# Performance work log

Measured on AMD Instinct MI355X. Metric: run time of the kernel, lower is better.

## Reference

```python
import jax, jax.numpy as jnp
import numpy as np

N, D_IN, D_OUT = 16384, 1024, 1024
E, R, TOP_K = 8, 16, 2
ALPHA = 32.0
SCALING = ALPHA / R  # standard LoRA scaling alpha/rank


def setup_inputs() -> dict:
    key = jax.random.key(0)
    k_tok, k_wb, k_a, k_b, k_g = jax.random.split(key, 5)
    tokens = jax.random.normal(k_tok, (N, D_IN), dtype=jnp.float32)
    # frozen attention projection
    W_base = jax.random.normal(k_wb, (D_IN, D_OUT), dtype=jnp.float32) * (1.0 / np.sqrt(D_IN))
    # per-expert LoRA factors
    A = jax.random.normal(k_a, (E, D_IN, R), dtype=jnp.float32) * 0.02
    B = jax.random.normal(k_b, (E, R, D_OUT), dtype=jnp.float32) * 0.02
    # router
    W_gate = jax.random.normal(k_g, (D_IN, E), dtype=jnp.float32) * (1.0 / np.sqrt(D_IN))
    return {"tokens": tokens, "W_base": W_base, "A": A, "B": B, "W_gate": W_gate}


def reference(tokens, W_base, A, B, W_gate):
    # Router: top-k gating with softmax over the selected logits
    router_logits = tokens @ W_gate                      # [N, E]
    topk_vals, selected_experts = jax.lax.top_k(router_logits, TOP_K)  # [N, K]
    expert_weights = jax.nn.softmax(topk_vals, axis=-1)  # [N, K]

    # Dense combine weights: zeros except selected experts
    gates = jnp.zeros((tokens.shape[0], E), dtype=tokens.dtype)
    gates = gates.at[jnp.arange(tokens.shape[0])[:, None], selected_experts].set(expert_weights)  # [N, E]

    # Frozen base projection
    base_out = tokens @ W_base                           # [N, D_out]

    # LoRA experts: low-rank intermediate [N, E, R] is small (rank 16)
    h = jnp.einsum('nd,edr->ner', tokens, A)             # [N, E, R]
    h = h * gates[:, :, None]                            # gate before expanding to D_out
    lora_out = jnp.einsum('ner,erm->nm', h, B)           # [N, D_out]

    out = base_out + SCALING * lora_out
    return out, router_logits, selected_experts, expert_weights
```

## Files before the change

kernel.cpp:

```cpp
#include <hip/hip_runtime.h>
#include <hip/hip_bf16.h>
#include <cstdint>
#include <cfloat>

#define NTOK 16384
#define DIN  1024
#define DOUT 1024
#define NEXP 8
#define RLORA 16
#define KTOT 1152
#define SCALE_LORA 2.0f

typedef __attribute__((ext_vector_type(8))) short bf16x8;
typedef __attribute__((ext_vector_type(4))) float f32x4;

__device__ __forceinline__ unsigned short f2bf(float f) {
  __hip_bfloat16 h = __float2bfloat16(f);
  unsigned short u;
  __builtin_memcpy(&u, &h, 2);
  return u;
}

__device__ __forceinline__ void gld_lds16(const void* g, void* l) {
  __builtin_amdgcn_global_load_lds((const __attribute__((address_space(1))) void*)g,
                                   (__attribute__((address_space(3))) void*)l,
                                   16, 0, 0);
}

__global__ __launch_bounds__(256) void k_prep(const float* __restrict__ Wb,
                                              const float* __restrict__ B,
                                              const float* __restrict__ A,
                                              const float* __restrict__ Wg,
                                              unsigned short* __restrict__ WcatT,
                                              unsigned short* __restrict__ AcatT,
                                              float* __restrict__ WgT) {
  __shared__ unsigned short Tbuf[256 * 17];
  const int bid = blockIdx.x;
  const int t = threadIdx.x;
  if (bid < 288) {
    unsigned short (*T)[66] = (unsigned short (*)[66])Tbuf;
    const int k0 = (bid % 18) * 64, j0 = (bid / 18) * 64;
#pragma unroll
    for (int p = 0; p < 4; ++p) {
      int kk = p * 16 + (t >> 4);
      int c4 = (t & 15) * 4;
      int k = k0 + kk;
      const float* src = (k < 1024) ? (Wb + (size_t)k * 1024) : (B + (size_t)(k - 1024) * 1024);
      float4 v = *(const float4*)(src + j0 + c4);
      T[kk][c4 + 0] = f2bf(v.x); T[kk][c4 + 1] = f2bf(v.y);
      T[kk][c4 + 2] = f2bf(v.z); T[kk][c4 + 3] = f2bf(v.w);
    }
    __syncthreads();
#pragma unroll
    for (int p = 0; p < 2; ++p) {
      int jj = p * 32 + (t >> 3);
      int kc = (t & 7) * 8;
      unsigned short buf[8];
#pragma unroll
      for (int i = 0; i < 8; ++i) buf[i] = T[kc + i][jj];
      uint4 u; __builtin_memcpy(&u, buf, 16);
      *(uint4*)(WcatT + (size_t)(j0 + jj) * KTOT + k0 + kc) = u;
    }
  } else if (bid < 320) {
    unsigned short (*T)[17] = (unsigned short (*)[17])Tbuf;
    const int e = (bid - 288) >> 2, d0 = ((bid - 288) & 3) * 256;
#pragma unroll
    for (int p = 0; p < 4; ++p) {
      int idx = p * 256 + t;
      int d = idx >> 2;
      int rr = (idx & 3) * 4;
      float4 v = *(const float4*)(A + (size_t)e * 16384 + (size_t)(d0 + d) * 16 + rr);
      T[d][rr + 0] = f2bf(v.x); T[d][rr + 1] = f2bf(v.y);
      T[d][rr + 2] = f2bf(v.z); T[d][rr + 3] = f2bf(v.w);
    }
    __syncthreads();
#pragma unroll
    for (int p = 0; p < 2; ++p) {
      int slot = p * 256 + t;
      int r = slot >> 5;
      int dc = (slot & 31) * 8;
      unsigned short buf[8];
#pragma unroll
      for (int i = 0; i < 8; ++i) buf[i] = T[dc + i][r];
      uint4 u; __builtin_memcpy(&u, buf, 16);
      *(uint4*)(AcatT + (size_t)(e * 16 + r) * 1024 + d0 + dc) = u;
    }
  } else {
    int d = (bid - 320) * 256 + t;
    float4 a = *(const float4*)(Wg + (size_t)d * 8);
    float4 b = *(const float4*)(Wg + (size_t)d * 8 + 4);
    WgT[0 * 1024 + d] = a.x; WgT[1 * 1024 + d] = a.y;
    WgT[2 * 1024 + d] = a.z; WgT[3 * 1024 + d] = a.w;
    WgT[4 * 1024 + d] = b.x; WgT[5 * 1024 + d] = b.y;
    WgT[6 * 1024 + d] = b.z; WgT[7 * 1024 + d] = b.w;
  }
}

__global__ __launch_bounds__(256) void k_router(const float* __restrict__ tokens,
                                                const float* __restrict__ WgT,
                                                float* __restrict__ out_logits,
                                                float* __restrict__ out_sel,
                                                float* __restrict__ out_w,
                                                unsigned short* __restrict__ Xcat,
                                                float4* __restrict__ gateinfo) {
  const int wid = threadIdx.x >> 6;
  const int lane = threadIdx.x & 63;
  const int t0 = (blockIdx.x * 4 + wid) * 2;

  float4 xa[4], xb[4];
  const float* x0 = tokens + (size_t)t0 * DIN;
  const float* x1 = x0 + DIN;
#pragma unroll
  for (int j = 0; j < 4; ++j) {
    xa[j] = *(const float4*)(x0 + j * 256 + lane * 4);
    xb[j] = *(const float4*)(x1 + j * 256 + lane * 4);
  }

#pragma unroll
  for (int tt = 0; tt < 2; ++tt) {
    unsigned short* xbp = Xcat + (size_t)(t0 + tt) * KTOT;
    const float4* xv = tt ? xb : xa;
#pragma unroll
    for (int j = 0; j < 4; ++j) {
      const float* xf = (const float*)&xv[j];
      unsigned short hb[4];
#pragma unroll
      for (int m = 0; m < 4; ++m) hb[m] = f2bf(xf[m]);
      uint2 u;
      __builtin_memcpy(&u, hb, 8);
      *(uint2*)(xbp + j * 256 + lane * 4) = u;
    }
  }

  float accA[8] = {0,0,0,0,0,0,0,0}, accB[8] = {0,0,0,0,0,0,0,0};
#pragma unroll
  for (int j = 0; j < 4; ++j) {
#pragma unroll
    for (int e = 0; e < 8; ++e) {
      float4 wv = *(const float4*)(WgT + (size_t)e * 1024 + j * 256 + lane * 4);
      accA[e] = fmaf(xa[j].x, wv.x, fmaf(xa[j].y, wv.y,
                fmaf(xa[j].z, wv.z, fmaf(xa[j].w, wv.w, accA[e]))));
      accB[e] = fmaf(xb[j].x, wv.x, fmaf(xb[j].y, wv.y,
                fmaf(xb[j].z, wv.z, fmaf(xb[j].w, wv.w, accB[e]))));
    }
  }
#pragma unroll
  for (int s = 1; s < 64; s <<= 1) {
#pragma unroll
    for (int e = 0; e < 8; ++e) {
      accA[e] += __shfl_xor(accA[e], s, 64);
      accB[e] += __shfl_xor(accB[e], s, 64);
    }
  }

#pragma unroll
  for (int tt = 0; tt < 2; ++tt) {
    const float* acc = tt ? accB : accA;
    int t = t0 + tt;
    float v0 = -FLT_MAX, v1 = -FLT_MAX;
    int i0 = -1, i1 = -1;
#pragma unroll
    for (int e = 0; e < 8; ++e) {
      float v = acc[e];
      if (v > v0) { v1 = v0; i1 = i0; v0 = v; i0 = e; }
      else if (v > v1) { v1 = v; i1 = e; }
    }
    float ex = expf(v1 - v0);
    float inv = 1.0f / (1.0f + ex);
    float w0 = inv, w1 = ex * inv;
    if (lane == 0) {
      float4* lg = (float4*)(out_logits + (size_t)t * 8);
      lg[0] = make_float4(acc[0], acc[1], acc[2], acc[3]);
      lg[1] = make_float4(acc[4], acc[5], acc[6], acc[7]);
      *(float2*)(out_sel + (size_t)t * 2) = make_float2((float)i0, (float)i1);
      *(float2*)(out_w + (size_t)t * 2) = make_float2(w0, w1);
      gateinfo[t] = make_float4((float)i0, (float)i1, w0 * SCALE_LORA, w1 * SCALE_LORA);
    }
  }
}

__global__ __launch_bounds__(256) void k_hgemm(const unsigned short* __restrict__ Xg,
                                               const unsigned short* __restrict__ Ag,
                                               const float4* __restrict__ gateinfo,
                                               unsigned short* __restrict__ Xout) {
  constexpr int BK = 64;
  __shared__ alignas(16) unsigned short As[64 * BK];
  __shared__ alignas(16) unsigned short Bs[64 * BK];
  const int tid = threadIdx.x;
  const int lane = tid & 63;
  const int wid = tid >> 6;
  const int id = blockIdx.x;
  const int xcd = id & 7, s5 = id >> 3;
  const int n0 = (s5 & 1) * 64;
  const int m0 = (xcd * 32 + (s5 >> 1)) * 64;
  const int wm = (wid >> 1) * 32, wn = (wid & 1) * 32;
  const int quad = lane >> 4, r16 = lane & 15;

  f32x4 acc[2][2] = {};

  for (int k0 = 0; k0 < 1024; k0 += BK) {
#pragma unroll
    for (int i = 0; i < 2; ++i) {
      int s = i * 256 + tid;
      int r = s >> 3, c = s & 7;
      int q = c ^ ((r >> 1) & 7);
      gld_lds16(Xg + (size_t)(m0 + r) * KTOT + k0 + q * 8, (char*)As + s * 16);
    }
#pragma unroll
    for (int i = 0; i < 2; ++i) {
      int s = i * 256 + tid;
      int r = s >> 3, c = s & 7;
      int q = c ^ ((r >> 1) & 7);
      gld_lds16(Ag + (size_t)(n0 + r) * 1024 + k0 + q * 8, (char*)Bs + s * 16);
    }
    __syncthreads();

#pragma unroll
    for (int h = 0; h < 2; ++h) {
      bf16x8 af[2], bfr[2];
#pragma unroll
      for (int mi = 0; mi < 2; ++mi) {
        int m = wm + mi * 16 + r16;
        int slot = m * 8 + ((h * 4 + quad) ^ ((m >> 1) & 7));
        af[mi] = *(const bf16x8*)((const char*)As + slot * 16);
      }
#pragma unroll
      for (int ni = 0; ni < 2; ++ni) {
        int n = wn + ni * 16 + r16;
        int slot = n * 8 + ((h * 4 + quad) ^ ((n >> 1) & 7));
        bfr[ni] = *(const bf16x8*)((const char*)Bs + slot * 16);
      }
#pragma unroll
      for (int mi = 0; mi < 2; ++mi)
#pragma unroll
        for (int ni = 0; ni < 2; ++ni)
          acc[mi][ni] = __builtin_amdgcn_mfma_f32_16x16x32_bf16(af[mi], bfr[ni], acc[mi][ni], 0, 0, 0);
    }
    __syncthreads();
  }

#pragma unroll
  for (int mi = 0; mi < 2; ++mi)
#pragma unroll
    for (int r = 0; r < 4; ++r) {
      int row = m0 + wm + mi * 16 + quad * 4 + r;
      float4 gi = gateinfo[row];
      int ie0 = (int)gi.x, ie1 = (int)gi.y;
#pragma unroll
      for (int ni = 0; ni < 2; ++ni) {
        int c = n0 + wn + ni * 16 + r16;
        int e = c >> 4;
        float h = acc[mi][ni][r];
        float v = (e == ie0) ? gi.z * h : ((e == ie1) ? gi.w * h : 0.f);
        Xout[(size_t)row * KTOT + 1024 + c] = f2bf(v);
      }
    }
}

__global__ __launch_bounds__(512, 2) void k_gemm_main(const unsigned short* __restrict__ Xg,
                                                      const unsigned short* __restrict__ Wgm,
                                                      float* __restrict__ C) {
  __shared__ alignas(16) unsigned short As[2][2][128 * 64];
  __shared__ alignas(16) unsigned short Bs[2][2][128 * 64];
  const int tid = threadIdx.x;
  const int lane = tid & 63;
  const int wid = tid >> 6;
  const int id = blockIdx.x;
  const int xcd = id & 7, loc = id >> 3;
  const int gid = xcd * 32 + loc;
  const int m0 = (gid >> 2) * 256;
  const int n0 = (gid & 3) * 256;
  const int wr64 = (wid >> 2) * 64;
  const int wc32 = (wid & 3) * 32;
  const int quad = lane >> 4, r16 = lane & 15;

  f32x4 acc[2][2][4][2] = {};

#define STAGE_A(SL, HF, KT)                                                   \
  {                                                                           \
    _Pragma("unroll")                                                         \
    for (int i_ = 0; i_ < 2; ++i_) {                                          \
      int s_ = i_ * 512 + tid;                                                \
      int r_ = s_ >> 3, c_ = s_ & 7;                                          \
      int q_ = c_ ^ ((r_ >> 1) & 7);                                          \
      gld_lds16(Xg + (size_t)(m0 + (HF) * 128 + r_) * KTOT + (KT) * 64 + q_ * 8, \
                (char*)As[SL][HF] + s_ * 16);                                 \
    }                                                                         \
  }
#define STAGE_B(SL, HF, KT)                                                   \
  {                                                                           \
    _Pragma("unroll")                                                         \
    for (int i_ = 0; i_ < 2; ++i_) {                                          \
      int s_ = i_ * 512 + tid;                                                \
      int r_ = s_ >> 3, c_ = s_ & 7;                                          \
      int q_ = c_ ^ ((r_ >> 1) & 7);                                          \
      gld_lds16(Wgm + (size_t)(n0 + (HF) * 128 + r_) * KTOT + (KT) * 64 + q_ * 8, \
                (char*)Bs[SL][HF] + s_ * 16);                                 \
    }                                                                         \
  }

#define PHASE(SL, MH, NH, ...)                                                \
  {                                                                           \
    bf16x8 af[4][2], bfr[2][2];                                               \
    const char* Ab = (const char*)As[SL][MH];                                 \
    const char* Bb = (const char*)Bs[SL][NH];                                 \
    _Pragma("unroll")                                                         \
    for (int mi = 0; mi < 4; ++mi) {                                          \
      int rh = wr64 + mi * 16 + r16;                                          \
      int sw = (rh >> 1) & 7;                                                 \
      af[mi][0] = *(const bf16x8*)(Ab + (rh * 8 + (quad ^ sw)) * 16);         \
      af[mi][1] = *(const bf16x8*)(Ab + (rh * 8 + ((4 + quad) ^ sw)) * 16);   \
    }                                                                         \
    _Pragma("unroll")                                                         \
    for (int ni = 0; ni < 2; ++ni) {                                          \
      int rh = wc32 + ni * 16 + r16;                                          \
      int sw = (rh >> 1) & 7;                                                 \
      bfr[ni][0] = *(const bf16x8*)(Bb + (rh * 8 + (quad ^ sw)) * 16);        \
      bfr[ni][1] = *(const bf16x8*)(Bb + (rh * 8 + ((4 + quad) ^ sw)) * 16);  \
    }                                                                         \
    __VA_ARGS__;                                                              \
    asm volatile("" ::: "memory");                                            \
    __builtin_amdgcn_s_barrier();                                             \
    asm volatile("s_waitcnt lgkmcnt(0)" ::: "memory");                        \
    __builtin_amdgcn_sched_barrier(0);                                        \
    __builtin_amdgcn_s_setprio(1);                                            \
    _Pragma("unroll")                                                         \
    for (int mi = 0; mi < 4; ++mi)                                            \
      _Pragma("unroll")                                                       \
      for (int ni = 0; ni < 2; ++ni) {                                        \
        acc[MH][NH][mi][ni] = __builtin_amdgcn_mfma_f32_16x16x32_bf16(        \
            af[mi][0], bfr[ni][0], acc[MH][NH][mi][ni], 0, 0, 0);             \
        acc[MH][NH][mi][ni] = __builtin_amdgcn_mfma_f32_16x16x32_bf16(        \
            af[mi][1], bfr[ni][1], acc[MH][NH][mi][ni], 0, 0, 0);             \
      }                                                                       \
    __builtin_amdgcn_s_setprio(0);                                            \
    asm volatile("" ::: "memory");                                            \
    __builtin_amdgcn_s_barrier();                                             \
  }

  STAGE_A(0, 0, 0); STAGE_A(0, 1, 0); STAGE_B(0, 0, 0); STAGE_B(0, 1, 0);
  STAGE_A(1, 1, 1);
  asm volatile("s_waitcnt vmcnt(2)" ::: "memory");
  __builtin_amdgcn_s_barrier();

  for (int it = 0; it < 9; ++it) {
    const int kt1 = 2 * it + 1;
    const int kt2 = (2 * it + 2 < 18) ? 2 * it + 2 : 17;
    const int kt3 = (2 * it + 3 < 18) ? 2 * it + 3 : 17;
    PHASE(0, 0, 0, STAGE_A(1, 0, kt1); STAGE_B(1, 0, kt1))
    PHASE(0, 1, 1, STAGE_B(1, 1, kt1))
    PHASE(0, 1, 0, )
    PHASE(0, 0, 1, STAGE_A(0, 1, kt2);
                   asm volatile("s_waitcnt vmcnt(2)" ::: "memory"))
    PHASE(1, 0, 0, STAGE_A(0, 0, kt2); STAGE_B(0, 0, kt2))
    PHASE(1, 1, 1, STAGE_B(0, 1, kt2))
    PHASE(1, 1, 0, )
    PHASE(1, 0, 1, STAGE_A(1, 1, kt3);
                   asm volatile("s_waitcnt vmcnt(2)" ::: "memory"))
  }
  asm volatile("s_waitcnt vmcnt(0)" ::: "memory");
#undef PHASE
#undef STAGE_A
#undef STAGE_B

#pragma unroll
  for (int mh = 0; mh < 2; ++mh)
#pragma unroll
    for (int nh = 0; nh < 2; ++nh)
#pragma unroll
      for (int mi = 0; mi < 4; ++mi)
#pragma unroll
        for (int ni = 0; ni < 2; ++ni)
#pragma unroll
          for (int r = 0; r < 4; ++r) {
            int row = m0 + mh * 128 + wr64 + mi * 16 + quad * 4 + r;
            int cc = n0 + nh * 128 + wc32 + ni * 16 + r16;
            C[(size_t)row * 1024 + cc] = acc[mh][nh][mi][ni][r];
          }
}

extern "C" void kernel_launch(void* const* d_in, const int* in_sizes, int n_in,
                              void* d_out, int out_size, void* d_ws, size_t ws_size,
                              hipStream_t stream) {
  const float* tokens = (const float*)d_in[0];
  const float* Wb     = (const float*)d_in[1];
  const float* A      = (const float*)d_in[2];
  const float* B      = (const float*)d_in[3];
  const float* Wg     = (const float*)d_in[4];
  float* out = (float*)d_out;

  char* ws = (char*)d_ws;
  unsigned short* Xcat  = (unsigned short*)(ws);
  unsigned short* WcatT = (unsigned short*)(ws + 37748736);
  unsigned short* AcatT = (unsigned short*)(ws + 40108032);
  float4*         ginfo = (float4*)(ws + 40370176);
  float*          WgT   = (float*)(ws + 40632320);

  float* out_logits = out + (size_t)16384 * 1024;
  float* out_sel    = out_logits + (size_t)16384 * 8;
  float* out_w      = out_sel + (size_t)16384 * 2;

  k_prep<<<dim3(324), dim3(256), 0, stream>>>(Wb, B, A, Wg, WcatT, AcatT, WgT);
  k_router<<<dim3(2048), dim3(256), 0, stream>>>(tokens, WgT, out_logits, out_sel, out_w, Xcat, ginfo);
  k_hgemm<<<dim3(512), dim3(256), 0, stream>>>(Xcat, AcatT, ginfo, Xcat);
  k_gemm_main<<<dim3(256), dim3(512), 0, stream>>>(Xcat, WcatT, out);
}
```

Baseline: 186.1 us.

## Reorder GEMM phases to reuse A/B register fragments across sub-tiles

Restructures the 8-phase main GEMM loop so LDS fragment reads for the next sub-tile are issued in a window before the MFMAs, and B fragments are double-buffered in registers (bf_a/bf_b). Phase order now walks the quadrants so either A or B fragments carry over between phases, which cuts redundant LDS reads. It also reorders the global-to-LDS staging and the vmcnt waits. The aim is to hide LDS latency and reduce LDS traffic, at the cost of more live registers and tighter ordering constraints between waits and staging.

```diff
diff --git a/kernel.cpp b/kernel.cpp
--- a/kernel.cpp
+++ b/kernel.cpp
@@ -275,6 +275,9 @@
   const int quad = lane >> 4, r16 = lane & 15;
 
   f32x4 acc[2][2][4][2] = {};
+  bf16x8 af[4][2];
+  bf16x8 bf_a[2][2];
+  bf16x8 bf_b[2][2];
 
 #define STAGE_A(SL, HF, KT)                                                   \
   {                                                                           \
@@ -298,70 +301,81 @@
                 (char*)Bs[SL][HF] + s_ * 16);                                 \
     }                                                                         \
   }
-
-#define PHASE(SL, MH, NH, ...)                                                \
+#define DS_A(SL, HF)                                                          \
   {                                                                           \
-    bf16x8 af[4][2], bfr[2][2];                                               \
-    const char* Ab = (const char*)As[SL][MH];                                 \
-    const char* Bb = (const char*)Bs[SL][NH];                                 \
     _Pragma("unroll")                                                         \
-    for (int mi = 0; mi < 4; ++mi) {                                          \
-      int rh = wr64 + mi * 16 + r16;                                          \
-      int sw = (rh >> 1) & 7;                                                 \
-      af[mi][0] = *(const bf16x8*)(Ab + (rh * 8 + (quad ^ sw)) * 16);         \
-      af[mi][1] = *(const bf16x8*)(Ab + (rh * 8 + ((4 + quad) ^ sw)) * 16);   \
+    for (int mi_ = 0; mi_ < 4; ++mi_) {                                       \
+      int rh_ = wr64 + mi_ * 16 + r16;                                        \
+      int sw_ = (rh_ >> 1) & 7;                                               \
+      af[mi_][0] = *(const bf16x8*)((const char*)As[SL][HF] +                 \
+                                    (rh_ * 8 + (quad ^ sw_)) * 16);           \
+      af[mi_][1] = *(const bf16x8*)((const char*)As[SL][HF] +                 \
+                                    (rh_ * 8 + ((4 + quad) ^ sw_)) * 16);     \
     }                                                                         \
+  }
+#define DS_B(DEST, SL, HF)                                                    \
+  {                                                                           \
     _Pragma("unroll")                                                         \
-    for (int ni = 0; ni < 2; ++ni) {                                          \
-      int rh = wc32 + ni * 16 + r16;                                          \
-      int sw = (rh >> 1) & 7;                                                 \
-      bfr[ni][0] = *(const bf16x8*)(Bb + (rh * 8 + (quad ^ sw)) * 16);        \
-      bfr[ni][1] = *(const bf16x8*)(Bb + (rh * 8 + ((4 + quad) ^ sw)) * 16);  \
+    for (int ni_ = 0; ni_ < 2; ++ni_) {                                       \
+      int rh_ = wc32 + ni_ * 16 + r16;                                        \
+      int sw_ = (rh_ >> 1) & 7;                                               \
+      DEST[ni_][0] = *(const bf16x8*)((const char*)Bs[SL][HF] +               \
+                                      (rh_ * 8 + (quad ^ sw_)) * 16);         \
+      DEST[ni_][1] = *(const bf16x8*)((const char*)Bs[SL][HF] +               \
+                                      (rh_ * 8 + ((4 + quad) ^ sw_)) * 16);   \
     }                                                                         \
-    __VA_ARGS__;                                                              \
+  }
+#define VM(N) asm volatile("s_waitcnt vmcnt(" #N ")" ::: "memory")
+
+#define PH(TOP, WIN, MH, NH, BF)                                              \
+  {                                                                           \
+    TOP;                                                                      \
     asm volatile("" ::: "memory");                                            \
     __builtin_amdgcn_s_barrier();                                             \
     asm volatile("s_waitcnt lgkmcnt(0)" ::: "memory");                        \
     __builtin_amdgcn_sched_barrier(0);                                        \
+    WIN;                                                                      \
+    __builtin_amdgcn_sched_barrier(0);                                        \
     __builtin_amdgcn_s_setprio(1);                                            \
     _Pragma("unroll")                                                         \
-    for (int mi = 0; mi < 4; ++mi)                                            \
+    for (int kk_ = 0; kk_ < 2; ++kk_)                                         \
       _Pragma("unroll")                                                       \
-      for (int ni = 0; ni < 2; ++ni) {                                        \
-        acc[MH][NH][mi][ni] = __builtin_amdgcn_mfma_f32_16x16x32_bf16(        \
-            af[mi][0], bfr[ni][0], acc[MH][NH][mi][ni], 0, 0, 0);             \
-        acc[MH][NH][mi][ni] = __builtin_amdgcn_mfma_f32_16x16x32_bf16(        \
-            af[mi][1], bfr[ni][1], acc[MH][NH][mi][ni], 0, 0, 0);             \
-      }                                                                       \
+      for (int mi_ = 0; mi_ < 4; ++mi_)                                       \
+        _Pragma("unroll")                                                     \
+        for (int ni_ = 0; ni_ < 2; ++ni_)                                     \
+          acc[MH][NH][mi_][ni_] = __builtin_amdgcn_mfma_f32_16x16x32_bf16(    \
+              af[mi_][kk_], BF[ni_][kk_], acc[MH][NH][mi_][ni_], 0, 0, 0);    \
     __builtin_amdgcn_s_setprio(0);                                            \
     asm volatile("" ::: "memory");                                            \
     __builtin_amdgcn_s_barrier();                                             \
   }
 
-  STAGE_A(0, 0, 0); STAGE_A(0, 1, 0); STAGE_B(0, 0, 0); STAGE_B(0, 1, 0);
-  STAGE_A(1, 1, 1);
-  asm volatile("s_waitcnt vmcnt(2)" ::: "memory");
+  STAGE_A(0, 0, 0); STAGE_B(0, 0, 0); STAGE_B(0, 1, 0); STAGE_A(0, 1, 0);
+  VM(2);
   __builtin_amdgcn_s_barrier();
+  DS_B(bf_a, 0, 0);
 
   for (int it = 0; it < 9; ++it) {
     const int kt1 = 2 * it + 1;
     const int kt2 = (2 * it + 2 < 18) ? 2 * it + 2 : 17;
-    const int kt3 = (2 * it + 3 < 18) ? 2 * it + 3 : 17;
-    PHASE(0, 0, 0, STAGE_A(1, 0, kt1); STAGE_B(1, 0, kt1))
-    PHASE(0, 1, 1, STAGE_B(1, 1, kt1))
-    PHASE(0, 1, 0, )
-    PHASE(0, 0, 1, STAGE_A(0, 1, kt2);
-                   asm volatile("s_waitcnt vmcnt(2)" ::: "memory"))
-    PHASE(1, 0, 0, STAGE_A(0, 0, kt2); STAGE_B(0, 0, kt2))
-    PHASE(1, 1, 1, STAGE_B(0, 1, kt2))
-    PHASE(1, 1, 0, )
-    PHASE(1, 0, 1, STAGE_A(1, 1, kt3);
-                   asm volatile("s_waitcnt vmcnt(2)" ::: "memory"))
-  }
-  asm volatile("s_waitcnt vmcnt(0)" ::: "memory");
-#undef PHASE
+    PH(DS_A(0, 0); STAGE_A(1, 0, kt1); STAGE_B(1, 0, kt1),
+       DS_B(bf_b, 0, 1), 0, 0, bf_a)
+    PH(STAGE_B(1, 1, kt1); VM(6), , 0, 1, bf_b)
+    PH(DS_A(0, 1), , 1, 1, bf_b)
+    PH(STAGE_A(1, 1, kt1); VM(2), DS_B(bf_b, 1, 0), 1, 0, bf_a)
+    PH(DS_A(1, 0); STAGE_A(0, 0, kt2); STAGE_B(0, 0, kt2),
+       DS_B(bf_a, 1, 1), 0, 0, bf_b)
+    PH(STAGE_B(0, 1, kt2); VM(6), , 0, 1, bf_a)
+    PH(DS_A(1, 1), , 1, 1, bf_a)
+    PH(STAGE_A(0, 1, kt2); VM(2), DS_B(bf_a, 0, 0), 1, 0, bf_b)
+  }
+  asm volatile("s_waitcnt vmcnt(0) lgkmcnt(0)" ::: "memory");
+#undef PH
+#undef VM
+#undef DS_B
+#undef DS_A
+#undef STAGE_B
 #undef STAGE_A
-#undef STAGE_B
 
 #pragma unroll
   for (int mh = 0; mh < 2; ++mh)
```

Result: slower. 190.0 us (+2.1%).
